# Kernel tuning notes

Hardware: AMD Instinct MI355X
Metric: run time of the kernel (lower is better)

## Reference

```python
import jax, jax.numpy as jnp
import numpy as np

N = 262144          # batch size
C = 100             # num_classes
R0, R1 = 0.95, 1.0  # recall_range
LAM = 0.5           # lambda_pauc
LS = 0.1            # label_smoothing
MAX_PAUC = R1 - R0


def setup_inputs() -> dict:
    key = jax.random.key(0)
    k1, k2 = jax.random.split(key)
    predictions = jax.random.normal(k1, (N, C), dtype=jnp.float32)
    targets = jax.random.randint(k2, (N,), 0, C)
    weight = jnp.ones((C,), dtype=jnp.float32)
    return {"predictions": predictions, "targets": targets, "weight": weight}


def _roc_curves(scores, labels):
    """Vectorized per-class ROC. scores, labels: [C, N].
    Replaces the O(N^2) per-threshold loop with sort + cumsum (tie-correct:
    tp at threshold s_j counts ALL samples with score >= s_j)."""
    order = jnp.argsort(-scores, axis=1)                      # descending
    ss = jnp.take_along_axis(scores, order, axis=1)           # [C, N]
    sl = jnp.take_along_axis(labels, order, axis=1)           # [C, N]
    cpos = jnp.cumsum(sl, axis=1)                             # cumulative positives
    # last index within each tie-group of equal scores
    neg = -ss  # ascending
    idx = jax.vmap(lambda a: jnp.searchsorted(a, a, side='right'))(neg) - 1
    tp = jnp.take_along_axis(cpos, idx, axis=1)
    cnt = (idx + 1).astype(scores.dtype)
    fp = cnt - tp
    P = cpos[:, -1:]                       # total positives per class
    Nn = scores.shape[1] - P               # total negatives per class
    tpr = jnp.where(P > 0, tp / jnp.maximum(P, 1.0), 0.0)
    fpr = jnp.where(Nn > 0, fp / jnp.maximum(Nn, 1.0), 0.0)
    return fpr, tpr


def reference(predictions, targets, weight):
    probs = jax.nn.softmax(predictions, axis=1)               # [N, C]
    onehot = jnp.eye(C, dtype=predictions.dtype)[targets]     # [N, C]
    onehot_s = (1.0 - LS) * onehot + LS / C

    # per-class binary labels (smoothed true-class value > 0.5)
    labels = (onehot_s > 0.5).astype(predictions.dtype).T     # [C, N]
    scores = probs.T                                          # [C, N]

    fpr, tpr = _roc_curves(scores, labels)
    mask = (tpr >= R0) & (tpr <= R1)
    y = jnp.maximum(tpr - R0, 0.0)
    # tpr is monotone non-decreasing, so the recall mask is contiguous and
    # trapz over the masked subset == sum over adjacent pairs both in mask.
    pm = (mask[:, :-1] & mask[:, 1:]).astype(predictions.dtype)
    pauc = jnp.sum(0.5 * (y[:, :-1] + y[:, 1:]) * (fpr[:, 1:] - fpr[:, :-1]) * pm, axis=1)  # [C]

    avg_p_auc = jnp.sum(pauc * weight) / (jnp.sum(weight) * MAX_PAUC)
    # torch computes TP/FP via .item(): the pAUC path carries no gradient
    avg_p_auc = jax.lax.stop_gradient(jnp.clip(avg_p_auc, 0.0, 1.0))

    log_probs = jax.nn.log_softmax(predictions, axis=1)
    ce_loss = -jnp.mean(jnp.sum(onehot_s * log_probs * weight, axis=1))
    pauc_loss = 1.0 - avg_p_auc ** 2
    return (1.0 - LAM) * ce_loss + LAM * pauc_loss
```

## Files before the change

kernel.cpp:

```cpp
#include <hip/hip_runtime.h>
#include <math.h>

#define WAVE 64
constexpr int   CC      = 100;
constexpr int   MAXM    = 160;
constexpr int   BUCKET  = 4096;
constexpr int   USTRIDE = 161;
constexpr int   LCAP    = 4096;
constexpr float LSMOOTH = 0.1f;
constexpr int   TILE    = 64;

__global__ __launch_bounds__(256) void k1_tile(
    const float* __restrict__ pred, const int* __restrict__ targets,
    const float* __restrict__ weight, float* __restrict__ L_out,
    float* __restrict__ pos_out, float* __restrict__ ce_partial, int N)
{
    __shared__ float tile[TILE * CC];
    __shared__ int   ttgt[TILE];
    __shared__ float tL[TILE], tpos[TILE];
    __shared__ float cered[4];
    const int tid = threadIdx.x;
    const int r0  = blockIdx.x * TILE;

    const float4* src = (const float4*)(pred + (size_t)r0 * CC);
    #pragma unroll
    for (int t = tid; t < TILE * (CC / 4); t += 256)
        *((float4*)&tile[t * 4]) = src[t];
    if (tid < TILE) ttgt[tid] = targets[r0 + tid];
    __syncthreads();

    const int x = tid & 15;
    const int G = tid >> 4;
    float w[7];
    #pragma unroll
    for (int j = 0; j < 7; ++j) {
        int c = x + 16 * j;
        w[j] = (c < CC) ? weight[c] : 0.0f;
    }
    float Wl = 0.0f;
    #pragma unroll
    for (int j = 0; j < 7; ++j) Wl += w[j];
    #pragma unroll
    for (int off = 1; off < 16; off <<= 1) Wl += __shfl_xor(Wl, off, 16);

    float ce_acc = 0.0f;
    #pragma unroll
    for (int rr = 0; rr < 4; ++rr) {
        const int r = G * 4 + rr;
        const float* rp = tile + r * CC;
        float v[7];
        #pragma unroll
        for (int j = 0; j < 7; ++j) {
            int c = x + 16 * j;
            v[j] = (c < CC) ? rp[c] : -INFINITY;
        }
        float vmax = v[0];
        #pragma unroll
        for (int j = 1; j < 7; ++j) vmax = fmaxf(vmax, v[j]);
        #pragma unroll
        for (int off = 1; off < 16; off <<= 1) vmax = fmaxf(vmax, __shfl_xor(vmax, off, 16));
        float z = 0.0f, ws = 0.0f;
        #pragma unroll
        for (int j = 0; j < 7; ++j) {
            int c = x + 16 * j;
            if (c < CC) { z += __expf(v[j] - vmax); ws += w[j] * v[j]; }
        }
        #pragma unroll
        for (int off = 1; off < 16; off <<= 1) {
            z  += __shfl_xor(z,  off, 16);
            ws += __shfl_xor(ws, off, 16);
        }
        float L = vmax + __logf(z);
        if (x == 0) {
            int t = ttgt[r];
            float pt = rp[t];
            tL[r] = L; tpos[r] = pt - L;
            ce_acc += -((1.0f - LSMOOTH) * weight[t] * (pt - L)
                        + (LSMOOTH / CC) * (ws - Wl * L));
        }
    }
    #pragma unroll
    for (int off = 32; off; off >>= 1) ce_acc += __shfl_xor(ce_acc, off, WAVE);
    if ((tid & 63) == 0) cered[tid >> 6] = ce_acc;
    __syncthreads();
    if (tid < TILE) {
        L_out[r0 + tid]   = tL[tid];
        pos_out[r0 + tid] = tpos[tid];
    }
    if (tid == 0)
        ce_partial[blockIdx.x] = cered[0] + cered[1] + cered[2] + cered[3];
}

__global__ __launch_bounds__(256) void k1b_scatter(
    const int* __restrict__ targets, const float* __restrict__ pos,
    int* __restrict__ cls_cnt, float* __restrict__ bucket, int N)
{
    __shared__ int hist[CC];
    __shared__ int base[CC];
    __shared__ int loc[CC];
    const int tid = threadIdx.x;
    const int rowsPerBlock = N / gridDim.x;
    const int r0 = blockIdx.x * rowsPerBlock;
    const int r1 = r0 + rowsPerBlock;
    for (int c = tid; c < CC; c += blockDim.x) { hist[c] = 0; loc[c] = 0; }
    __syncthreads();
    for (int r = r0 + tid; r < r1; r += blockDim.x)
        atomicAdd(&hist[targets[r]], 1);
    __syncthreads();
    for (int c = tid; c < CC; c += blockDim.x)
        base[c] = (hist[c] > 0) ? atomicAdd(&cls_cnt[c], hist[c]) : 0;
    __syncthreads();
    for (int r = r0 + tid; r < r1; r += blockDim.x) {
        int c = targets[r];
        int idx = base[c] + atomicAdd(&loc[c], 1);
        if (idx < BUCKET) bucket[(size_t)c * BUCKET + idx] = pos[r];
    }
}

__global__ __launch_bounds__(256) void k2_select(
    const float* __restrict__ bucket, const int* __restrict__ cls_cnt,
    float* __restrict__ u, int* __restrict__ m_arr, int* __restrict__ P_arr,
    float* __restrict__ wm_arr)
{
    __shared__ unsigned int keys[BUCKET];
    __shared__ unsigned int hist[256];
    __shared__ unsigned int scan[256];
    __shared__ unsigned int sel[256];
    __shared__ unsigned int s_prefix;
    __shared__ int s_rank;
    __shared__ int cnt_lt;
    const int c   = blockIdx.x;
    const int tid = threadIdx.x;
    const int P = min(cls_cnt[c], BUCKET);
    double Kd = 0.95 * (double)P;
    int kf = (int)floor(Kd);
    int m = P - kf;
    if (m > MAXM) m = MAXM;
    if (m < 0) m = 0;
    if (tid == 0) {
        m_arr[c] = m; P_arr[c] = P;
        wm_arr[c] = (float)((double)(kf + 1) - Kd);
        s_prefix = 0; s_rank = m - 1; cnt_lt = 0;
    }
    for (int i = tid; i < P; i += 256) {
        unsigned int b = __float_as_uint(bucket[(size_t)c * BUCKET + i]);
        keys[i] = (b & 0x80000000u) ? ~b : (b | 0x80000000u);
    }
    __syncthreads();
    if (m == 0) return;

    for (int shift = 24; shift >= 0; shift -= 8) {
        hist[tid] = 0;
        __syncthreads();
        unsigned int pref = s_prefix;
        for (int i = tid; i < P; i += 256) {
            unsigned int k = keys[i];
            bool match = (shift == 24) || ((k >> (shift + 8)) == pref);
            if (match) atomicAdd(&hist[(k >> shift) & 255u], 1u);
        }
        __syncthreads();
        scan[tid] = hist[tid];
        __syncthreads();
        for (int off = 1; off < 256; off <<= 1) {
            unsigned int add = (tid >= off) ? scan[tid - off] : 0u;
            __syncthreads();
            scan[tid] += add;
            __syncthreads();
        }
        int r = s_rank;
        unsigned int inc = scan[tid];
        unsigned int exc = inc - hist[tid];
        __syncthreads();
        if ((unsigned int)r >= exc && (unsigned int)r < inc) {
            s_rank   = r - (int)exc;
            s_prefix = (pref << 8) | (unsigned int)tid;
        }
        __syncthreads();
    }
    const unsigned int kth = s_prefix;

    for (int i = tid; i < P; i += 256) {
        unsigned int k = keys[i];
        if (k < kth) {
            int pslot = atomicAdd(&cnt_lt, 1);
            sel[pslot] = k;
        }
    }
    __syncthreads();
    const int nlt = cnt_lt;
    for (int j = nlt + tid; j < 256; j += 256) sel[j] = (j < m) ? kth : 0xFFFFFFFFu;
    __syncthreads();
    for (int kk = 2; kk <= 256; kk <<= 1) {
        for (int j = kk >> 1; j > 0; j >>= 1) {
            int i = tid, ixj = tid ^ j;
            if (ixj > i) {
                unsigned int a = sel[i], b = sel[ixj];
                bool up = ((i & kk) == 0);
                if ((a > b) == up) { sel[i] = b; sel[ixj] = a; }
            }
            __syncthreads();
        }
    }
    if (tid < m) {
        unsigned int k = sel[tid];
        unsigned int b = (k & 0x80000000u) ? (k & 0x7fffffffu) : ~k;
        u[c * MAXM + tid] = __uint_as_float(b);
    }
}

__device__ __forceinline__ int ubound(const float* uc, int m, float key, int maxidx) {
    int l = 0;
    #pragma unroll
    for (int s = 128; s; s >>= 1) {
        int p = l + s - 1;
        float val = uc[p < maxidx ? p : maxidx];
        l += ((p < m) && (val <= key)) ? s : 0;
    }
    return l;
}

__global__ __launch_bounds__(256) void k3a_stream(
    const float4* __restrict__ pred4, const float* __restrict__ L,
    const float* __restrict__ u, const int* __restrict__ m_arr,
    uint2* __restrict__ list, int* __restrict__ list_cnt, int list_cap,
    int* __restrict__ g_cnt, int* __restrict__ g_sum, int total4)
{
    __shared__ float umax_s[CC];
    __shared__ uint2 buf[LCAP];
    __shared__ int lcnt;
    __shared__ int gbase;
    const int tid = threadIdx.x;
    if (tid < CC) {
        int m = m_arr[tid];
        umax_s[tid] = (m > 0) ? u[tid * MAXM + m - 1] : -INFINITY;
    }
    if (tid == 0) lcnt = 0;
    __syncthreads();

    const int stride = gridDim.x * blockDim.x;
    int i = blockIdx.x * blockDim.x + tid;
    int j = i % 25;
    int n = i / 25;
    const int dj = stride % 25, dn = stride / 25;
    while (i < total4) {
        float4 v = pred4[i];
        float Ln = L[n];
        float4 um = *((const float4*)&umax_s[j * 4]);
        float s0 = v.x - Ln, s1 = v.y - Ln, s2 = v.z - Ln, s3 = v.w - Ln;
        #pragma unroll
        for (int q = 0; q < 4; ++q) {
            float sc = (q == 0) ? s0 : (q == 1) ? s1 : (q == 2) ? s2 : s3;
            float mx = (q == 0) ? um.x : (q == 1) ? um.y : (q == 2) ? um.z : um.w;
            if (sc < mx) {
                int c = j * 4 + q;
                int idx = atomicAdd(&lcnt, 1);
                if (idx < LCAP) {
                    buf[idx] = make_uint2((unsigned int)c, __float_as_uint(sc));
                } else {
                    int m = m_arr[c];
                    int l = ubound(u + c * MAXM, m, sc, MAXM - 1);
                    atomicAdd(&g_cnt[c], 1);
                    atomicAdd(&g_sum[c], m - 1 - l);
                }
            }
        }
        i += stride; j += dj; n += dn;
        if (j >= 25) { j -= 25; n += 1; }
    }
    __syncthreads();
    int cnt = min(lcnt, LCAP);
    if (tid == 0) gbase = atomicAdd(list_cnt, cnt);
    __syncthreads();
    const int base0 = gbase;
    for (int k = tid; k < cnt; k += 256) {
        int gi = base0 + k;
        if (gi < list_cap) {
            list[gi] = buf[k];
        } else {
            uint2 e = buf[k];
            int c = (int)e.x; float sc = __uint_as_float(e.y);
            int m = m_arr[c];
            int l = ubound(u + c * MAXM, m, sc, MAXM - 1);
            atomicAdd(&g_cnt[c], 1);
            atomicAdd(&g_sum[c], m - 1 - l);
        }
    }
}

__global__ __launch_bounds__(256) void k3b_rank(
    const uint2* __restrict__ list, const int* __restrict__ list_cnt, int list_cap,
    const float* __restrict__ u, const int* __restrict__ m_arr,
    int* __restrict__ g_cnt, int* __restrict__ g_sum)
{
    __shared__ float us[CC * USTRIDE];
    __shared__ int sm[CC];
    __shared__ int lcnt[CC], lsum[CC];
    const int tid = threadIdx.x;
    for (int c = tid; c < CC; c += 256) { sm[c] = m_arr[c]; lcnt[c] = 0; lsum[c] = 0; }
    for (int t = tid; t < CC * MAXM; t += 256) {
        int c = t / MAXM, k = t - c * MAXM;
        us[c * USTRIDE + k] = u[t];
    }
    __syncthreads();
    const int n = min(*list_cnt, list_cap);
    const int stride = gridDim.x * blockDim.x;
    for (int idx = blockIdx.x * blockDim.x + tid; idx < n; idx += stride) {
        uint2 e = list[idx];
        int c = (int)e.x;
        float key = __uint_as_float(e.y);
        int m = sm[c];
        int l = ubound(us + c * USTRIDE, m, key, USTRIDE - 1);
        atomicAdd(&lcnt[c], 1);
        atomicAdd(&lsum[c], m - 1 - l);
    }
    __syncthreads();
    for (int c = tid; c < CC; c += 256) {
        if (lcnt[c]) { atomicAdd(&g_cnt[c], lcnt[c]); atomicAdd(&g_sum[c], lsum[c]); }
    }
}

__global__ __launch_bounds__(256) void k4_final(
    const float* __restrict__ ce_partial, int nPartial,
    const float* __restrict__ weight, const int* __restrict__ P_arr,
    const int* __restrict__ m_arr, const float* __restrict__ wm_arr,
    const int* __restrict__ g_cnt, const int* __restrict__ g_sum,
    float* __restrict__ out, int N)
{
    __shared__ double r1[256], r2[256], r3[256];
    double ce = 0.0;
    for (int i = threadIdx.x; i < nPartial; i += blockDim.x) ce += (double)ce_partial[i];
    double p = 0.0, wsum = 0.0;
    for (int c = threadIdx.x; c < CC; c += blockDim.x) {
        int P = P_arr[c], m = m_arr[c];
        double wgt = (double)weight[c];
        long long Nn = (long long)N - P;
        if (P > 0 && Nn > 0 && m > 0) {
            double wm = (double)wm_arr[c];
            double S   = (double)g_sum[c] + wm * (double)g_cnt[c];
            double sub = 0.5 * (double)(m - 1) * (double)(m - 2) + wm * (double)(m - 1);
            double pc  = (S - sub) / ((double)Nn * (double)P);
            if (pc < 0.0) pc = 0.0;
            p += pc * wgt;
        }
        wsum += wgt;
    }
    r1[threadIdx.x] = ce; r2[threadIdx.x] = p; r3[threadIdx.x] = wsum;
    __syncthreads();
    for (int off = blockDim.x >> 1; off; off >>= 1) {
        if ((int)threadIdx.x < off) {
            r1[threadIdx.x] += r1[threadIdx.x + off];
            r2[threadIdx.x] += r2[threadIdx.x + off];
            r3[threadIdx.x] += r3[threadIdx.x + off];
        }
        __syncthreads();
    }
    if (threadIdx.x == 0) {
        double ce_loss = r1[0] / (double)N;
        double avg = r2[0] / (r3[0] * 0.05);
        avg = fmin(fmax(avg, 0.0), 1.0);
        out[0] = (float)(0.5 * ce_loss + 0.5 * (1.0 - avg * avg));
    }
}

extern "C" void kernel_launch(void* const* d_in, const int* in_sizes, int n_in,
                              void* d_out, int out_size, void* d_ws, size_t ws_size,
                              hipStream_t stream) {
    (void)n_in; (void)out_size;
    const float* pred    = (const float*)d_in[0];
    const int*   targets = (const int*)d_in[1];
    const float* weight  = (const float*)d_in[2];
    float* out = (float*)d_out;
    const int N = in_sizes[1];

    const int K1_BLOCKS = N / TILE;
    char* base = (char*)d_ws;
    size_t off = 0;
    auto take = [&](size_t bytes) { char* q = base + off; off += (bytes + 15) & ~(size_t)15; return q; };
    float* L_ws       = (float*)take((size_t)N * 4);
    float* pos_ws     = (float*)take((size_t)N * 4);
    float* ce_partial = (float*)take((size_t)K1_BLOCKS * 4);
    float* u          = (float*)take((size_t)CC * MAXM * 4);
    int*   m_arr      = (int*)take(CC * 4);
    int*   P_arr      = (int*)take(CC * 4);
    float* wm_arr     = (float*)take(CC * 4);
    int*   zero_blk   = (int*)take(304 * 4);
    int*   cls_cnt  = zero_blk;
    int*   g_cnt    = zero_blk + CC;
    int*   g_sum    = zero_blk + 2 * CC;
    int*   list_cnt = zero_blk + 3 * CC;
    float* bucket     = (float*)take((size_t)CC * BUCKET * 4);
    uint2* list       = (uint2*)(base + off);
    long long rem     = (long long)ws_size - (long long)off;
    int list_cap      = (rem > 0) ? (int)(rem / 8) : 0;

    hipMemsetAsync(zero_blk, 0, 304 * 4, stream);

    k1_tile<<<K1_BLOCKS, 256, 0, stream>>>(pred, targets, weight, L_ws, pos_ws,
                                           ce_partial, N);
    k1b_scatter<<<256, 256, 0, stream>>>(targets, pos_ws, cls_cnt, bucket, N);
    k2_select<<<CC, 256, 0, stream>>>(bucket, cls_cnt, u, m_arr, P_arr, wm_arr);
    const int total4 = (int)((size_t)N * CC / 4);
    k3a_stream<<<1024, 256, 0, stream>>>((const float4*)pred, L_ws, u, m_arr,
                                         list, list_cnt, list_cap, g_cnt, g_sum, total4);
    k3b_rank<<<512, 256, 0, stream>>>(list, list_cnt, list_cap, u, m_arr, g_cnt, g_sum);
    k4_final<<<1, 256, 0, stream>>>(ce_partial, K1_BLOCKS, weight, P_arr, m_arr, wm_arr,
                                    g_cnt, g_sum, out, N);
}
```

Measured before the change: 263.5 us.

## Fuse all stages into one persistent kernel with grid barriers

Replaces six kernel launches with a single persistent 512-block kernel that moves between phases through atomic-counter grid barriers. Phase 1 double-buffers row tiles into LDS via global_load_lds and scatters per-class positive scores directly from a shared pair buffer, so the separate pos array and scatter kernel go away. It also swaps the select stage's shared-memory scan for a wave shuffle scan and lowers MAXM to 152. The aim is to remove launch gaps and extra global traffic, at the risk of a deadlock if all 512 blocks cannot be co-resident, with serialization at each barrier, and with the select phase using only 100 of the blocks.

Measured after the change: 544.3 us. 107% more time.

```diff
diff --git a/kernel.cpp b/kernel.cpp
--- a/kernel.cpp
+++ b/kernel.cpp
@@ -3,57 +3,137 @@
 
 #define WAVE 64
 constexpr int   CC      = 100;
-constexpr int   MAXM    = 160;
+constexpr int   MAXM    = 152;
+constexpr int   USTRIDE = 153;
 constexpr int   BUCKET  = 4096;
-constexpr int   USTRIDE = 161;
 constexpr int   LCAP    = 4096;
+constexpr int   PAIRCAP = 640;
 constexpr float LSMOOTH = 0.1f;
 constexpr int   TILE    = 64;
-
-__global__ __launch_bounds__(256) void k1_tile(
+constexpr int   GRID    = 512;
+constexpr int   NTHR    = 256;
+constexpr int   T4TILE  = TILE * CC / 4;
+
+struct P1S {
+  float  tile[2][TILE * CC];
+  float  tL[2][TILE];
+  uint2  pairs[PAIRCAP];
+  int    hist[CC], loc[CC], basec[CC];
+  double cered[4];
+  int    paircnt;
+};
+struct P2S {
+  unsigned keys[BUCKET];
+  unsigned hist[256], scan[256], sel[256];
+  unsigned prefix;
+  int rank, cnt_lt;
+};
+struct P3S {
+  float umax[CC];
+  uint2 buf[LCAP];
+  int lcnt, gbase;
+};
+struct P4S {
+  float us[CC * USTRIDE];
+  int sm[CC], lcnt[CC], lsum[CC];
+};
+struct P5S { double r1[NTHR], r2[NTHR], r3[NTHR]; };
+union SH { P1S p1; P2S p2; P3S p3; P4S p4; P5S p5; };
+
+__device__ __forceinline__ void gload_lds16(const void* g, void* lds) {
+  __builtin_amdgcn_global_load_lds(
+      (const __attribute__((address_space(1))) void*)g,
+      (__attribute__((address_space(3))) void*)lds, 16, 0, 0);
+}
+
+__device__ __forceinline__ void stage_tile(float* dst, const float4* src) {
+  int t = (int)threadIdx.x;
+  #pragma unroll
+  for (int k = 0; k < T4TILE / NTHR; ++k) {
+    gload_lds16((const void*)(src + t), (char*)dst + (size_t)t * 16);
+    t += NTHR;
+  }
+  if (t < T4TILE)
+    gload_lds16((const void*)(src + t), (char*)dst + (size_t)t * 16);
+}
+
+__device__ __forceinline__ void grid_barrier(int* bar, int phase) {
+  __threadfence();
+  __syncthreads();
+  if (threadIdx.x == 0) {
+    atomicAdd(bar, 1);
+    const int target = GRID * phase;
+    while (__hip_atomic_load(bar, __ATOMIC_ACQUIRE, __HIP_MEMORY_SCOPE_AGENT) < target)
+      __builtin_amdgcn_s_sleep(2);
+  }
+  __syncthreads();
+}
+
+__device__ __forceinline__ int ubound(const float* uc, int m, float key, int maxidx) {
+  int l = 0;
+  #pragma unroll
+  for (int s = 128; s; s >>= 1) {
+    int p = l + s - 1;
+    float val = uc[p < maxidx ? p : maxidx];
+    l += ((p < m) && (val <= key)) ? s : 0;
+  }
+  return l;
+}
+
+__global__ __launch_bounds__(NTHR, 2) void mega(
     const float* __restrict__ pred, const int* __restrict__ targets,
-    const float* __restrict__ weight, float* __restrict__ L_out,
-    float* __restrict__ pos_out, float* __restrict__ ce_partial, int N)
+    const float* __restrict__ weight, float* __restrict__ out,
+    float* __restrict__ L_ws, double* __restrict__ ce_blk,
+    float* __restrict__ u, int* __restrict__ m_arr, int* __restrict__ P_arr,
+    float* __restrict__ wm_arr, int* __restrict__ zb,
+    float* __restrict__ bucket, uint2* __restrict__ list,
+    int list_cap, int N)
 {
-    __shared__ float tile[TILE * CC];
-    __shared__ int   ttgt[TILE];
-    __shared__ float tL[TILE], tpos[TILE];
-    __shared__ float cered[4];
-    const int tid = threadIdx.x;
-    const int r0  = blockIdx.x * TILE;
-
-    const float4* src = (const float4*)(pred + (size_t)r0 * CC);
-    #pragma unroll
-    for (int t = tid; t < TILE * (CC / 4); t += 256)
-        *((float4*)&tile[t * 4]) = src[t];
-    if (tid < TILE) ttgt[tid] = targets[r0 + tid];
-    __syncthreads();
+  __shared__ __align__(16) SH sh;
+  const int tid = (int)threadIdx.x;
+  const int bid = (int)blockIdx.x;
+  int* cls_cnt  = zb;
+  int* g_cnt    = zb + CC;
+  int* g_sum    = zb + 2 * CC;
+  int* list_cnt = zb + 3 * CC;
+  int* bar      = zb + 3 * CC + 1;
+
+  {
+    const int ntiles = N / TILE;
+    stage_tile(sh.p1.tile[0], (const float4*)(pred + (size_t)bid * TILE * CC));
+    for (int c2 = tid; c2 < CC; c2 += NTHR) { sh.p1.hist[c2] = 0; sh.p1.loc[c2] = 0; }
+    if (tid == 0) sh.p1.paircnt = 0;
 
     const int x = tid & 15;
     const int G = tid >> 4;
     float w[7];
     #pragma unroll
-    for (int j = 0; j < 7; ++j) {
-        int c = x + 16 * j;
-        w[j] = (c < CC) ? weight[c] : 0.0f;
-    }
+    for (int j = 0; j < 7; ++j) { int c2 = x + 16 * j; w[j] = (c2 < CC) ? weight[c2] : 0.0f; }
     float Wl = 0.0f;
     #pragma unroll
     for (int j = 0; j < 7; ++j) Wl += w[j];
     #pragma unroll
     for (int off = 1; off < 16; off <<= 1) Wl += __shfl_xor(Wl, off, 16);
 
-    float ce_acc = 0.0f;
-    #pragma unroll
-    for (int rr = 0; rr < 4; ++rr) {
+    asm volatile("s_waitcnt vmcnt(0)" ::: "memory");
+    __syncthreads();
+
+    double ce_acc = 0.0;
+    int it = 0;
+    for (int tt = bid; tt < ntiles; tt += GRID, ++it) {
+      const int cur = it & 1, nxt = cur ^ 1;
+      const int ttn = tt + GRID;
+      if (ttn < ntiles)
+        stage_tile(sh.p1.tile[nxt], (const float4*)(pred + (size_t)ttn * TILE * CC));
+
+      const int r0 = tt * TILE;
+      #pragma unroll
+      for (int rr = 0; rr < 4; ++rr) {
         const int r = G * 4 + rr;
-        const float* rp = tile + r * CC;
+        const float* rp = sh.p1.tile[cur] + r * CC;
         float v[7];
         #pragma unroll
-        for (int j = 0; j < 7; ++j) {
-            int c = x + 16 * j;
-            v[j] = (c < CC) ? rp[c] : -INFINITY;
-        }
+        for (int j = 0; j < 7; ++j) { int c2 = x + 16 * j; v[j] = (c2 < CC) ? rp[c2] : -INFINITY; }
         float vmax = v[0];
         #pragma unroll
         for (int j = 1; j < 7; ++j) vmax = fmaxf(vmax, v[j]);
@@ -62,75 +142,57 @@
         float z = 0.0f, ws = 0.0f;
         #pragma unroll
         for (int j = 0; j < 7; ++j) {
-            int c = x + 16 * j;
-            if (c < CC) { z += __expf(v[j] - vmax); ws += w[j] * v[j]; }
+          int c2 = x + 16 * j;
+          if (c2 < CC) { z += __expf(v[j] - vmax); ws += w[j] * v[j]; }
         }
         #pragma unroll
         for (int off = 1; off < 16; off <<= 1) {
-            z  += __shfl_xor(z,  off, 16);
-            ws += __shfl_xor(ws, off, 16);
-        }
-        float L = vmax + __logf(z);
+          z  += __shfl_xor(z,  off, 16);
+          ws += __shfl_xor(ws, off, 16);
+        }
         if (x == 0) {
-            int t = ttgt[r];
-            float pt = rp[t];
-            tL[r] = L; tpos[r] = pt - L;
-            ce_acc += -((1.0f - LSMOOTH) * weight[t] * (pt - L)
-                        + (LSMOOTH / CC) * (ws - Wl * L));
-        }
-    }
+          int tg = targets[r0 + r];
+          float pt = rp[tg];
+          float L = vmax + __logf(z);
+          sh.p1.tL[cur][r] = L;
+          float pos = pt - L;
+          int slot = atomicAdd(&sh.p1.paircnt, 1);
+          if (slot < PAIRCAP) {
+            sh.p1.pairs[slot] = make_uint2((unsigned)tg, __float_as_uint(pos));
+            atomicAdd(&sh.p1.hist[tg], 1);
+          } else {
+            int idx = atomicAdd(&cls_cnt[tg], 1);
+            if (idx < BUCKET) bucket[(size_t)tg * BUCKET + idx] = pos;
+          }
+          ce_acc += -(double)((1.0f - LSMOOTH) * weight[tg] * (pt - L)
+                              + (LSMOOTH / CC) * (ws - Wl * L));
+        }
+      }
+      asm volatile("s_waitcnt vmcnt(0)" ::: "memory");
+      __syncthreads();
+      if (tid < TILE) L_ws[r0 + tid] = sh.p1.tL[cur][tid];
+    }
+
     #pragma unroll
     for (int off = 32; off; off >>= 1) ce_acc += __shfl_xor(ce_acc, off, WAVE);
-    if ((tid & 63) == 0) cered[tid >> 6] = ce_acc;
-    __syncthreads();
-    if (tid < TILE) {
-        L_out[r0 + tid]   = tL[tid];
-        pos_out[r0 + tid] = tpos[tid];
-    }
+    if ((tid & 63) == 0) sh.p1.cered[tid >> 6] = ce_acc;
+    for (int c2 = tid; c2 < CC; c2 += NTHR)
+      sh.p1.basec[c2] = sh.p1.hist[c2] ? atomicAdd(&cls_cnt[c2], sh.p1.hist[c2]) : 0;
+    __syncthreads();
     if (tid == 0)
-        ce_partial[blockIdx.x] = cered[0] + cered[1] + cered[2] + cered[3];
-}
-
-__global__ __launch_bounds__(256) void k1b_scatter(
-    const int* __restrict__ targets, const float* __restrict__ pos,
-    int* __restrict__ cls_cnt, float* __restrict__ bucket, int N)
-{
-    __shared__ int hist[CC];
-    __shared__ int base[CC];
-    __shared__ int loc[CC];
-    const int tid = threadIdx.x;
-    const int rowsPerBlock = N / gridDim.x;
-    const int r0 = blockIdx.x * rowsPerBlock;
-    const int r1 = r0 + rowsPerBlock;
-    for (int c = tid; c < CC; c += blockDim.x) { hist[c] = 0; loc[c] = 0; }
-    __syncthreads();
-    for (int r = r0 + tid; r < r1; r += blockDim.x)
-        atomicAdd(&hist[targets[r]], 1);
-    __syncthreads();
-    for (int c = tid; c < CC; c += blockDim.x)
-        base[c] = (hist[c] > 0) ? atomicAdd(&cls_cnt[c], hist[c]) : 0;
-    __syncthreads();
-    for (int r = r0 + tid; r < r1; r += blockDim.x) {
-        int c = targets[r];
-        int idx = base[c] + atomicAdd(&loc[c], 1);
-        if (idx < BUCKET) bucket[(size_t)c * BUCKET + idx] = pos[r];
-    }
-}
-
-__global__ __launch_bounds__(256) void k2_select(
-    const float* __restrict__ bucket, const int* __restrict__ cls_cnt,
-    float* __restrict__ u, int* __restrict__ m_arr, int* __restrict__ P_arr,
-    float* __restrict__ wm_arr)
-{
-    __shared__ unsigned int keys[BUCKET];
-    __shared__ unsigned int hist[256];
-    __shared__ unsigned int scan[256];
-    __shared__ unsigned int sel[256];
-    __shared__ unsigned int s_prefix;
-    __shared__ int s_rank;
-    __shared__ int cnt_lt;
-    const int c   = blockIdx.x;
-    const int tid = threadIdx.x;
+      ce_blk[bid] = sh.p1.cered[0] + sh.p1.cered[1] + sh.p1.cered[2] + sh.p1.cered[3];
+    const int npair = min(sh.p1.paircnt, PAIRCAP);
+    for (int e = tid; e < npair; e += NTHR) {
+      uint2 pr = sh.p1.pairs[e];
+      int c2 = (int)pr.x;
+      int idx = sh.p1.basec[c2] + atomicAdd(&sh.p1.loc[c2], 1);
+      if (idx < BUCKET) bucket[(size_t)c2 * BUCKET + idx] = __uint_as_float(pr.y);
+    }
+  }
+  grid_barrier(bar, 1);
+
+  if (bid < CC) {
+    const int c = bid;
     const int P = min(cls_cnt[c], BUCKET);
     double Kd = 0.95 * (double)P;
     int kf = (int)floor(Kd);
@@ -138,271 +200,249 @@
     if (m > MAXM) m = MAXM;
     if (m < 0) m = 0;
     if (tid == 0) {
-        m_arr[c] = m; P_arr[c] = P;
-        wm_arr[c] = (float)((double)(kf + 1) - Kd);
-        s_prefix = 0; s_rank = m - 1; cnt_lt = 0;
-    }
-    for (int i = tid; i < P; i += 256) {
-        unsigned int b = __float_as_uint(bucket[(size_t)c * BUCKET + i]);
-        keys[i] = (b & 0x80000000u) ? ~b : (b | 0x80000000u);
-    }
-    __syncthreads();
-    if (m == 0) return;
-
-    for (int shift = 24; shift >= 0; shift -= 8) {
-        hist[tid] = 0;
+      m_arr[c] = m; P_arr[c] = P;
+      wm_arr[c] = (float)((double)(kf + 1) - Kd);
+      sh.p2.prefix = 0; sh.p2.rank = m - 1; sh.p2.cnt_lt = 0;
+    }
+    for (int i = tid; i < P; i += NTHR) {
+      unsigned b = __float_as_uint(bucket[(size_t)c * BUCKET + i]);
+      sh.p2.keys[i] = (b & 0x80000000u) ? ~b : (b | 0x80000000u);
+    }
+    __syncthreads();
+    if (m > 0) {
+      for (int shift = 24; shift >= 0; shift -= 8) {
+        sh.p2.hist[tid] = 0;
         __syncthreads();
-        unsigned int pref = s_prefix;
-        for (int i = tid; i < P; i += 256) {
-            unsigned int k = keys[i];
-            bool match = (shift == 24) || ((k >> (shift + 8)) == pref);
-            if (match) atomicAdd(&hist[(k >> shift) & 255u], 1u);
+        unsigned pref = sh.p2.prefix;
+        for (int i = tid; i < P; i += NTHR) {
+          unsigned k = sh.p2.keys[i];
+          bool match = (shift == 24) || ((k >> (shift + 8)) == pref);
+          if (match) atomicAdd(&sh.p2.hist[(k >> shift) & 255u], 1u);
         }
         __syncthreads();
-        scan[tid] = hist[tid];
+        if (tid < 64) {
+          unsigned h0 = sh.p2.hist[tid*4], h1 = sh.p2.hist[tid*4+1],
+                   h2 = sh.p2.hist[tid*4+2], h3 = sh.p2.hist[tid*4+3];
+          unsigned s0 = h0, s1 = s0 + h1, s2 = s1 + h2, s3 = s2 + h3;
+          unsigned sc = s3;
+          #pragma unroll
+          for (int off = 1; off < 64; off <<= 1) {
+            unsigned t2 = __shfl_up(sc, (unsigned)off, 64);
+            if (tid >= off) sc += t2;
+          }
+          unsigned excl = sc - s3;
+          sh.p2.scan[tid*4]   = excl + s0;
+          sh.p2.scan[tid*4+1] = excl + s1;
+          sh.p2.scan[tid*4+2] = excl + s2;
+          sh.p2.scan[tid*4+3] = excl + s3;
+        }
         __syncthreads();
-        for (int off = 1; off < 256; off <<= 1) {
-            unsigned int add = (tid >= off) ? scan[tid - off] : 0u;
-            __syncthreads();
-            scan[tid] += add;
-            __syncthreads();
-        }
-        int r = s_rank;
-        unsigned int inc = scan[tid];
-        unsigned int exc = inc - hist[tid];
+        int r = sh.p2.rank;
+        unsigned inc = sh.p2.scan[tid];
+        unsigned exc = inc - sh.p2.hist[tid];
         __syncthreads();
-        if ((unsigned int)r >= exc && (unsigned int)r < inc) {
-            s_rank   = r - (int)exc;
-            s_prefix = (pref << 8) | (unsigned int)tid;
+        if ((unsigned)r >= exc && (unsigned)r < inc) {
+          sh.p2.rank   = r - (int)exc;
+          sh.p2.prefix = (pref << 8) | (unsigned)tid;
         }
         __syncthreads();
-    }
-    const unsigned int kth = s_prefix;
-
-    for (int i = tid; i < P; i += 256) {
-        unsigned int k = keys[i];
-        if (k < kth) {
-            int pslot = atomicAdd(&cnt_lt, 1);
-            sel[pslot] = k;
-        }
-    }
-    __syncthreads();
-    const int nlt = cnt_lt;
-    for (int j = nlt + tid; j < 256; j += 256) sel[j] = (j < m) ? kth : 0xFFFFFFFFu;
-    __syncthreads();
-    for (int kk = 2; kk <= 256; kk <<= 1) {
-        for (int j = kk >> 1; j > 0; j >>= 1) {
-            int i = tid, ixj = tid ^ j;
-            if (ixj > i) {
-                unsigned int a = sel[i], b = sel[ixj];
-                bool up = ((i & kk) == 0);
-                if ((a > b) == up) { sel[i] = b; sel[ixj] = a; }
-            }
-            __syncthreads();
-        }
-    }
-    if (tid < m) {
-        unsigned int k = sel[tid];
-        unsigned int b = (k & 0x80000000u) ? (k & 0x7fffffffu) : ~k;
-        u[c * MAXM + tid] = __uint_as_float(b);
-    }
-}
-
-__device__ __forceinline__ int ubound(const float* uc, int m, float key, int maxidx) {
-    int l = 0;
-    #pragma unroll
-    for (int s = 128; s; s >>= 1) {
-        int p = l + s - 1;
-        float val = uc[p < maxidx ? p : maxidx];
-        l += ((p < m) && (val <= key)) ? s : 0;
-    }
-    return l;
-}
-
-__global__ __launch_bounds__(256) void k3a_stream(
-    const float4* __restrict__ pred4, const float* __restrict__ L,
-    const float* __restrict__ u, const int* __restrict__ m_arr,
-    uint2* __restrict__ list, int* __restrict__ list_cnt, int list_cap,
-    int* __restrict__ g_cnt, int* __restrict__ g_sum, int total4)
-{
-    __shared__ float umax_s[CC];
-    __shared__ uint2 buf[LCAP];
-    __shared__ int lcnt;
-    __shared__ int gbase;
-    const int tid = threadIdx.x;
+      }
+      const unsigned kth = sh.p2.prefix;
+      for (int i = tid; i < P; i += NTHR) {
+        unsigned k = sh.p2.keys[i];
+        if (k < kth) sh.p2.sel[atomicAdd(&sh.p2.cnt_lt, 1)] = k;
+      }
+      __syncthreads();
+      const int nlt = sh.p2.cnt_lt;
+      for (int j2 = nlt + tid; j2 < 256; j2 += NTHR)
+        sh.p2.sel[j2] = (j2 < m) ? kth : 0xFFFFFFFFu;
+      __syncthreads();
+      for (int kk = 2; kk <= 256; kk <<= 1)
+        for (int j2 = kk >> 1; j2 > 0; j2 >>= 1) {
+          int i2 = tid, ixj = tid ^ j2;
+          if (ixj > i2) {
+            unsigned a = sh.p2.sel[i2], b2 = sh.p2.sel[ixj];
+            bool up = ((i2 & kk) == 0);
+            if ((a > b2) == up) { sh.p2.sel[i2] = b2; sh.p2.sel[ixj] = a; }
+          }
+          __syncthreads();
+        }
+      if (tid < m) {
+        unsigned k = sh.p2.sel[tid];
+        unsigned b2 = (k & 0x80000000u) ? (k & 0x7fffffffu) : ~k;
+        u[c * MAXM + tid] = __uint_as_float(b2);
+      }
+    }
+  }
+  grid_barrier(bar, 2);
+
+  {
     if (tid < CC) {
-        int m = m_arr[tid];
-        umax_s[tid] = (m > 0) ? u[tid * MAXM + m - 1] : -INFINITY;
-    }
-    if (tid == 0) lcnt = 0;
-    __syncthreads();
-
-    const int stride = gridDim.x * blockDim.x;
-    int i = blockIdx.x * blockDim.x + tid;
-    int j = i % 25;
-    int n = i / 25;
-    const int dj = stride % 25, dn = stride / 25;
+      int m2 = m_arr[tid];
+      sh.p3.umax[tid] = (m2 > 0) ? u[tid * MAXM + m2 - 1] : -INFINITY;
+    }
+    if (tid == 0) sh.p3.lcnt = 0;
+    __syncthreads();
+    const float4* pred4 = (const float4*)pred;
+    const int total4 = N * (CC / 4);
+    const int stride = GRID * NTHR;
+
+    auto proc = [&](float4 v, float Ln, float4 um, int j) {
+      float s0 = v.x - Ln, s1 = v.y - Ln, s2 = v.z - Ln, s3 = v.w - Ln;
+      #pragma unroll
+      for (int q = 0; q < 4; ++q) {
+        float scv = (q == 0) ? s0 : (q == 1) ? s1 : (q == 2) ? s2 : s3;
+        float mx  = (q == 0) ? um.x : (q == 1) ? um.y : (q == 2) ? um.z : um.w;
+        if (scv < mx) {
+          int c2 = j * 4 + q;
+          int idx = atomicAdd(&sh.p3.lcnt, 1);
+          if (idx < LCAP) sh.p3.buf[idx] = make_uint2((unsigned)c2, __float_as_uint(scv));
+          else {
+            int m2 = m_arr[c2];
+            int l = ubound(u + c2 * MAXM, m2, scv, MAXM - 1);
+            atomicAdd(&g_cnt[c2], 1);
+            atomicAdd(&g_sum[c2], m2 - 1 - l);
+          }
+        }
+      }
+    };
+
+    int i = bid * NTHR + tid;
     while (i < total4) {
-        float4 v = pred4[i];
-        float Ln = L[n];
-        float4 um = *((const float4*)&umax_s[j * 4]);
-        float s0 = v.x - Ln, s1 = v.y - Ln, s2 = v.z - Ln, s3 = v.w - Ln;
-        #pragma unroll
-        for (int q = 0; q < 4; ++q) {
-            float sc = (q == 0) ? s0 : (q == 1) ? s1 : (q == 2) ? s2 : s3;
-            float mx = (q == 0) ? um.x : (q == 1) ? um.y : (q == 2) ? um.z : um.w;
-            if (sc < mx) {
-                int c = j * 4 + q;
-                int idx = atomicAdd(&lcnt, 1);
-                if (idx < LCAP) {
-                    buf[idx] = make_uint2((unsigned int)c, __float_as_uint(sc));
-                } else {
-                    int m = m_arr[c];
-                    int l = ubound(u + c * MAXM, m, sc, MAXM - 1);
-                    atomicAdd(&g_cnt[c], 1);
-                    atomicAdd(&g_sum[c], m - 1 - l);
-                }
-            }
-        }
-        i += stride; j += dj; n += dn;
-        if (j >= 25) { j -= 25; n += 1; }
-    }
-    __syncthreads();
-    int cnt = min(lcnt, LCAP);
-    if (tid == 0) gbase = atomicAdd(list_cnt, cnt);
-    __syncthreads();
-    const int base0 = gbase;
-    for (int k = tid; k < cnt; k += 256) {
-        int gi = base0 + k;
-        if (gi < list_cap) {
-            list[gi] = buf[k];
-        } else {
-            uint2 e = buf[k];
-            int c = (int)e.x; float sc = __uint_as_float(e.y);
-            int m = m_arr[c];
-            int l = ubound(u + c * MAXM, m, sc, MAXM - 1);
-            atomicAdd(&g_cnt[c], 1);
-            atomicAdd(&g_sum[c], m - 1 - l);
-        }
-    }
-}
-
-__global__ __launch_bounds__(256) void k3b_rank(
-    const uint2* __restrict__ list, const int* __restrict__ list_cnt, int list_cap,
-    const float* __restrict__ u, const int* __restrict__ m_arr,
-    int* __restrict__ g_cnt, int* __restrict__ g_sum)
-{
-    __shared__ float us[CC * USTRIDE];
-    __shared__ int sm[CC];
-    __shared__ int lcnt[CC], lsum[CC];
-    const int tid = threadIdx.x;
-    for (int c = tid; c < CC; c += 256) { sm[c] = m_arr[c]; lcnt[c] = 0; lsum[c] = 0; }
-    for (int t = tid; t < CC * MAXM; t += 256) {
-        int c = t / MAXM, k = t - c * MAXM;
-        us[c * USTRIDE + k] = u[t];
-    }
-    __syncthreads();
-    const int n = min(*list_cnt, list_cap);
-    const int stride = gridDim.x * blockDim.x;
-    for (int idx = blockIdx.x * blockDim.x + tid; idx < n; idx += stride) {
-        uint2 e = list[idx];
-        int c = (int)e.x;
-        float key = __uint_as_float(e.y);
-        int m = sm[c];
-        int l = ubound(us + c * USTRIDE, m, key, USTRIDE - 1);
-        atomicAdd(&lcnt[c], 1);
-        atomicAdd(&lsum[c], m - 1 - l);
-    }
-    __syncthreads();
-    for (int c = tid; c < CC; c += 256) {
-        if (lcnt[c]) { atomicAdd(&g_cnt[c], lcnt[c]); atomicAdd(&g_sum[c], lsum[c]); }
-    }
-}
-
-__global__ __launch_bounds__(256) void k4_final(
-    const float* __restrict__ ce_partial, int nPartial,
-    const float* __restrict__ weight, const int* __restrict__ P_arr,
-    const int* __restrict__ m_arr, const float* __restrict__ wm_arr,
-    const int* __restrict__ g_cnt, const int* __restrict__ g_sum,
-    float* __restrict__ out, int N)
-{
-    __shared__ double r1[256], r2[256], r3[256];
+      int i2 = i + stride;
+      bool has2 = (i2 < total4);
+      float4 v0 = pred4[i];
+      float4 v1 = has2 ? pred4[i2] : make_float4(0.f, 0.f, 0.f, 0.f);
+      int n0 = i / 25, j0 = i - n0 * 25;
+      float L0 = L_ws[n0];
+      float4 um0 = *(const float4*)&sh.p3.umax[j0 * 4];
+      proc(v0, L0, um0, j0);
+      if (has2) {
+        int n1 = i2 / 25, j1 = i2 - n1 * 25;
+        float L1 = L_ws[n1];
+        float4 um1 = *(const float4*)&sh.p3.umax[j1 * 4];
+        proc(v1, L1, um1, j1);
+      }
+      i += 2 * stride;
+    }
+    __syncthreads();
+    int cnt = min(sh.p3.lcnt, LCAP);
+    if (tid == 0) sh.p3.gbase = atomicAdd(list_cnt, cnt);
+    __syncthreads();
+    const int base0 = sh.p3.gbase;
+    for (int k2 = tid; k2 < cnt; k2 += NTHR) {
+      int gi = base0 + k2;
+      if (gi < list_cap) list[gi] = sh.p3.buf[k2];
+      else {
+        uint2 e = sh.p3.buf[k2];
+        int c2 = (int)e.x; float scv = __uint_as_float(e.y);
+        int m2 = m_arr[c2];
+        int l = ubound(u + c2 * MAXM, m2, scv, MAXM - 1);
+        atomicAdd(&g_cnt[c2], 1);
+        atomicAdd(&g_sum[c2], m2 - 1 - l);
+      }
+    }
+  }
+  grid_barrier(bar, 3);
+
+  {
+    for (int c2 = tid; c2 < CC; c2 += NTHR) {
+      sh.p4.sm[c2] = m_arr[c2]; sh.p4.lcnt[c2] = 0; sh.p4.lsum[c2] = 0;
+    }
+    for (int t = tid; t < CC * MAXM; t += NTHR) {
+      int c2 = t / MAXM, k2 = t - c2 * MAXM;
+      sh.p4.us[c2 * USTRIDE + k2] = u[t];
+    }
+    __syncthreads();
+    const int n2 = min(*list_cnt, list_cap);
+    const int stride = GRID * NTHR;
+    for (int idx = bid * NTHR + tid; idx < n2; idx += stride) {
+      uint2 e = list[idx];
+      int c2 = (int)e.x;
+      float key = __uint_as_float(e.y);
+      int m2 = sh.p4.sm[c2];
+      int l = ubound(sh.p4.us + c2 * USTRIDE, m2, key, USTRIDE - 1);
+      atomicAdd(&sh.p4.lcnt[c2], 1);
+      atomicAdd(&sh.p4.lsum[c2], m2 - 1 - l);
+    }
+    __syncthreads();
+    for (int c2 = tid; c2 < CC; c2 += NTHR)
+      if (sh.p4.lcnt[c2]) {
+        atomicAdd(&g_cnt[c2], sh.p4.lcnt[c2]);
+        atomicAdd(&g_sum[c2], sh.p4.lsum[c2]);
+      }
+  }
+  grid_barrier(bar, 4);
+
+  if (bid == 0) {
     double ce = 0.0;
-    for (int i = threadIdx.x; i < nPartial; i += blockDim.x) ce += (double)ce_partial[i];
+    for (int i2 = tid; i2 < GRID; i2 += NTHR) ce += ce_blk[i2];
     double p = 0.0, wsum = 0.0;
-    for (int c = threadIdx.x; c < CC; c += blockDim.x) {
-        int P = P_arr[c], m = m_arr[c];
-        double wgt = (double)weight[c];
-        long long Nn = (long long)N - P;
-        if (P > 0 && Nn > 0 && m > 0) {
-            double wm = (double)wm_arr[c];
-            double S   = (double)g_sum[c] + wm * (double)g_cnt[c];
-            double sub = 0.5 * (double)(m - 1) * (double)(m - 2) + wm * (double)(m - 1);
-            double pc  = (S - sub) / ((double)Nn * (double)P);
-            if (pc < 0.0) pc = 0.0;
-            p += pc * wgt;
-        }
-        wsum += wgt;
-    }
-    r1[threadIdx.x] = ce; r2[threadIdx.x] = p; r3[threadIdx.x] = wsum;
-    __syncthreads();
-    for (int off = blockDim.x >> 1; off; off >>= 1) {
-        if ((int)threadIdx.x < off) {
-            r1[threadIdx.x] += r1[threadIdx.x + off];
-            r2[threadIdx.x] += r2[threadIdx.x + off];
-            r3[threadIdx.x] += r3[threadIdx.x + off];
-        }
-        __syncthreads();
-    }
-    if (threadIdx.x == 0) {
-        double ce_loss = r1[0] / (double)N;
-        double avg = r2[0] / (r3[0] * 0.05);
-        avg = fmin(fmax(avg, 0.0), 1.0);
-        out[0] = (float)(0.5 * ce_loss + 0.5 * (1.0 - avg * avg));
-    }
+    for (int c2 = tid; c2 < CC; c2 += NTHR) {
+      int P = P_arr[c2], m2 = m_arr[c2];
+      double wgt = (double)weight[c2];
+      long long Nn = (long long)N - P;
+      if (P > 0 && Nn > 0 && m2 > 0) {
+        double wm = (double)wm_arr[c2];
+        double S   = (double)g_sum[c2] + wm * (double)g_cnt[c2];
+        double sub = 0.5 * (double)(m2 - 1) * (double)(m2 - 2) + wm * (double)(m2 - 1);
+        double pc  = (S - sub) / ((double)Nn * (double)P);
+        if (pc < 0.0) pc = 0.0;
+        p += pc * wgt;
+      }
+      wsum += wgt;
+    }
+    sh.p5.r1[tid] = ce; sh.p5.r2[tid] = p; sh.p5.r3[tid] = wsum;
+    __syncthreads();
+    for (int off = NTHR >> 1; off; off >>= 1) {
+      if (tid < off) {
+        sh.p5.r1[tid] += sh.p5.r1[tid + off];
+        sh.p5.r2[tid] += sh.p5.r2[tid + off];
+        sh.p5.r3[tid] += sh.p5.r3[tid + off];
+      }
+      __syncthreads();
+    }
+    if (tid == 0) {
+      double ce_loss = sh.p5.r1[0] / (double)N;
+      double avg = sh.p5.r2[0] / (sh.p5.r3[0] * 0.05);
+      avg = fmin(fmax(avg, 0.0), 1.0);
+      out[0] = (float)(0.5 * ce_loss + 0.5 * (1.0 - avg * avg));
+    }
+  }
 }
 
 extern "C" void kernel_launch(void* const* d_in, const int* in_sizes, int n_in,
                               void* d_out, int out_size, void* d_ws, size_t ws_size,
                               hipStream_t stream) {
-    (void)n_in; (void)out_size;
-    const float* pred    = (const float*)d_in[0];
-    const int*   targets = (const int*)d_in[1];
-    const float* weight  = (const float*)d_in[2];
-    float* out = (float*)d_out;
-    const int N = in_sizes[1];
-
-    const int K1_BLOCKS = N / TILE;
-    char* base = (char*)d_ws;
-    size_t off = 0;
-    auto take = [&](size_t bytes) { char* q = base + off; off += (bytes + 15) & ~(size_t)15; return q; };
-    float* L_ws       = (float*)take((size_t)N * 4);
-    float* pos_ws     = (float*)take((size_t)N * 4);
-    float* ce_partial = (float*)take((size_t)K1_BLOCKS * 4);
-    float* u          = (float*)take((size_t)CC * MAXM * 4);
-    int*   m_arr      = (int*)take(CC * 4);
-    int*   P_arr      = (int*)take(CC * 4);
-    float* wm_arr     = (float*)take(CC * 4);
-    int*   zero_blk   = (int*)take(304 * 4);
-    int*   cls_cnt  = zero_blk;
-    int*   g_cnt    = zero_blk + CC;
-    int*   g_sum    = zero_blk + 2 * CC;
-    int*   list_cnt = zero_blk + 3 * CC;
-    float* bucket     = (float*)take((size_t)CC * BUCKET * 4);
-    uint2* list       = (uint2*)(base + off);
-    long long rem     = (long long)ws_size - (long long)off;
-    int list_cap      = (rem > 0) ? (int)(rem / 8) : 0;
-
-    hipMemsetAsync(zero_blk, 0, 304 * 4, stream);
-
-    k1_tile<<<K1_BLOCKS, 256, 0, stream>>>(pred, targets, weight, L_ws, pos_ws,
-                                           ce_partial, N);
-    k1b_scatter<<<256, 256, 0, stream>>>(targets, pos_ws, cls_cnt, bucket, N);
-    k2_select<<<CC, 256, 0, stream>>>(bucket, cls_cnt, u, m_arr, P_arr, wm_arr);
-    const int total4 = (int)((size_t)N * CC / 4);
-    k3a_stream<<<1024, 256, 0, stream>>>((const float4*)pred, L_ws, u, m_arr,
-                                         list, list_cnt, list_cap, g_cnt, g_sum, total4);
-    k3b_rank<<<512, 256, 0, stream>>>(list, list_cnt, list_cap, u, m_arr, g_cnt, g_sum);
-    k4_final<<<1, 256, 0, stream>>>(ce_partial, K1_BLOCKS, weight, P_arr, m_arr, wm_arr,
-                                    g_cnt, g_sum, out, N);
-}
+  (void)n_in; (void)out_size;
+  const float* pred    = (const float*)d_in[0];
+  const int*   targets = (const int*)d_in[1];
+  const float* weight  = (const float*)d_in[2];
+  float* out = (float*)d_out;
+  const int N = in_sizes[1];
+
+  char* base = (char*)d_ws;
+  size_t off = 0;
+  auto take = [&](size_t bytes) {
+    char* q = base + off; off += (bytes + 15) & ~(size_t)15; return q;
+  };
+  float*  L_ws   = (float*)take((size_t)N * 4);
+  double* ce_blk = (double*)take((size_t)GRID * 8);
+  float*  u      = (float*)take((size_t)CC * MAXM * 4);
+  int*    m_arr  = (int*)take(CC * 4);
+  int*    P_arr  = (int*)take(CC * 4);
+  float*  wm_arr = (float*)take(CC * 4);
+  int*    zb     = (int*)take(312 * 4);
+  float*  bucket = (float*)take((size_t)CC * BUCKET * 4);
+  uint2*  list   = (uint2*)(base + off);
+  long long rem  = (long long)ws_size - (long long)off;
+  int list_cap   = (rem > 0) ? (int)(rem / 8) : 0;
+
+  hipMemsetAsync(zb, 0, 312 * 4, stream);
+
+  int list_cap_v = list_cap;
+  int N_v = N;
+  mega<<<dim3(GRID), dim3(NTHR), 0, stream>>>(
+      pred, targets, weight, out, L_ws, ce_blk, u, m_arr, P_arr, wm_arr,
+      zb, bucket, list, list_cap_v, N_v);
+}
```
